# Performance work log

Hardware: AMD Instinct MI355X
Metric: run time of the kernel (lower is better)

## Reference

```python
import jax, jax.numpy as jnp
import numpy as np

N_NODES = 100000

def gcn_conv(x, W, b, src, dst, n_nodes):
    # x: [N, Fin], W: [Fin, Fout], b: [Fout]; src/dst include self-loops.
    h = x @ W                                            # [N, Fout]
    deg = jnp.zeros((n_nodes,), x.dtype).at[dst].add(1.0)  # in-degree incl. self-loop
    dinv = jax.lax.rsqrt(deg)                            # deg >= 1 due to self-loops
    norm = dinv[src] * dinv[dst]                         # [E']
    msg = h[src] * norm[:, None]                         # [E', Fout]
    out = jax.ops.segment_sum(msg, dst, num_segments=n_nodes)
    return out + b

def setup_inputs() -> dict:
    key = jax.random.key(0)
    k1, k2, k3, k4, k5, k6 = jax.random.split(key, 6)
    in_c, hid_c, out_c = 128, 64, 32
    x = jax.random.normal(k1, (N_NODES, in_c), dtype=jnp.float32)
    edge_index = jax.random.randint(k2, (2, 1600000), 0, N_NODES, dtype=jnp.int64)
    # Glorot-ish init for weights
    W1 = jax.random.normal(k3, (in_c, hid_c), dtype=jnp.float32) / np.sqrt(in_c)
    b1 = jnp.zeros((hid_c,), dtype=jnp.float32)
    W2 = jax.random.normal(k4, (hid_c, out_c), dtype=jnp.float32) / np.sqrt(hid_c)
    b2 = jnp.zeros((out_c,), dtype=jnp.float32)
    return {"x": x, "edge_index": edge_index, "W1": W1, "b1": b1, "W2": W2, "b2": b2}

def reference(x, edge_index, W1, b1, W2, b2):
    n = x.shape[0]
    loops = jnp.arange(n, dtype=edge_index.dtype)
    src = jnp.concatenate([edge_index[0], loops])   # add self-loops
    dst = jnp.concatenate([edge_index[1], loops])
    h = gcn_conv(x, W1, b1, src, dst, n)
    h = jax.nn.relu(h)
    out = gcn_conv(h, W2, b2, src, dst, n)
    return out
```

## Files before the change

kernel.cpp:

```cpp
#include <hip/hip_runtime.h>
#include <hip/hip_bf16.h>


#define FIN1 128
#define FOUT1 64
#define FOUT2 32
#define PAD 64
#define NPB 200
#define NBUCKET 500
#define CAP 4096
#define EPB 4096

typedef unsigned int uint;
typedef unsigned short ushort;
typedef __attribute__((ext_vector_type(8))) short bf16x8;
typedef __attribute__((ext_vector_type(4))) float f32x4;

__device__ __forceinline__ ushort f2bf(float f) {
    uint u = __float_as_uint(f);
    return (ushort)((u + 0x7fffu + ((u >> 16) & 1u)) >> 16);
}
__device__ __forceinline__ float bf2f(ushort b) {
    return __uint_as_float(((uint)b) << 16);
}


__global__ __launch_bounds__(256) void bin_edges(const int* __restrict__ src,
                                                 const int* __restrict__ dst,
                                                 int* __restrict__ cursors,
                                                 int* __restrict__ binned, int e) {
    __shared__ int s_hist[NBUCKET];
    __shared__ int s_base[NBUCKET];
    __shared__ int s_cur[NBUCKET];
    const int t = threadIdx.x;
    for (int i = t; i < NBUCKET; i += 256) s_hist[i] = 0;
    __syncthreads();
    const int base = blockIdx.x * EPB;
    int vpk[16], vb[16];
#pragma unroll
    for (int k = 0; k < 16; ++k) {
        int idx = base + t + k * 256;
        bool ok = idx < e;
        int s = ok ? src[idx] : 0;
        int d = ok ? dst[idx] : 0;
        int bk = d / NPB;
        vb[k] = ok ? bk : -1;
        vpk[k] = s | ((d - bk * NPB) << 17);
        if (ok) atomicAdd(&s_hist[bk], 1);
    }
    __syncthreads();
    for (int i = t; i < NBUCKET; i += 256) {
        int h = s_hist[i];
        s_base[i] = (h > 0) ? atomicAdd(&cursors[i], h) : 0;
        s_cur[i] = 0;
    }
    __syncthreads();
#pragma unroll
    for (int k = 0; k < 16; ++k) {
        int bk = vb[k];
        if (bk >= 0) {
            int r = s_base[bk] + atomicAdd(&s_cur[bk], 1);
            if (r < CAP) binned[(size_t)bk * CAP + r] = vpk[k];
        }
    }
}


__global__ __launch_bounds__(256) void build_ell(const int* __restrict__ binned,
                                                 const int* __restrict__ cursors,
                                                 int* __restrict__ counts,
                                                 float* __restrict__ dinv,
                                                 int* __restrict__ ell, int n) {
    __shared__ int s_cnt[NPB];
    __shared__ int s_ell[NPB * PAD];
    const int b = blockIdx.x, t = threadIdx.x;
    for (int i = t; i < NPB; i += 256) s_cnt[i] = 0;
    {
        int4 pv = make_int4(n, n, n, n);
        int4* s4 = (int4*)s_ell;
        for (int i = t; i < NPB * PAD / 4; i += 256) s4[i] = pv;
    }
    __syncthreads();
    const int len = min(cursors[b], CAP);
    const int* edges = binned + (size_t)b * CAP;
    const int node0 = b * NPB;
    for (int i = t; i < len; i += 256) {
        int pk = edges[i];
        int local = pk >> 17;
        int r = atomicAdd(&s_cnt[local], 1);
        if (r < PAD) s_ell[local * PAD + r] = pk & 0x1FFFF;
    }
    __syncthreads();
    for (int i = t; i < NPB; i += 256) {
        int node = node0 + i;
        if (node < n) {
            int full = s_cnt[i];
            counts[node] = min((full + 7) & ~7, PAD);
            dinv[node] = rsqrtf((float)full + 1.0f);
        }
    }
    int4* d4 = (int4*)(ell + (size_t)node0 * PAD);
    const int4* s4 = (const int4*)s_ell;
    for (int i = t; i < NPB * PAD / 4; i += 256) d4[i] = s4[i];
}

template <int K, int F, int CT, int LOG2F>
__device__ __forceinline__ void stage_W(const float* __restrict__ W, ushort* sB, int t) {
    for (int sidx = t; sidx < K * F; sidx += 256) {
        int k = sidx >> LOG2F;
        int f = sidx & (F - 1);
        int kc = k >> 5, j = k & 7, quadb = (k >> 3) & 3;
        int c = f >> 4, nn = f & 15;
        int d = ((kc * CT + c) * 64 + quadb * 16 + nn) * 8 + j;
        sB[d] = f2bf(W[sidx]);
    }
}


template <int K, int F, int LOG2F>
__global__ __launch_bounds__(256) void gemm_mfma(const float* __restrict__ A,
                                                 const float* __restrict__ W,
                                                 const float* __restrict__ dinv,
                                                 ushort* __restrict__ out, int n) {
    constexpr int KC = K / 32;
    constexpr int CT = F / 16;
    __shared__ ushort sB[KC * CT * 64 * 8];
    const int t = threadIdx.x;
    stage_W<K, F, CT, LOG2F>(W, sB, t);
    __syncthreads();

    const int w = threadIdx.x >> 6;
    const int lane = threadIdx.x & 63;
    const int quad = lane >> 4;
    const int mcol = lane & 15;

    bf16x8 bfr[KC][CT];
    const bf16x8* sB8 = reinterpret_cast<const bf16x8*>(sB);
#pragma unroll
    for (int kc = 0; kc < KC; ++kc)
#pragma unroll
        for (int c = 0; c < CT; ++c)
            bfr[kc][c] = sB8[(kc * CT + c) * 64 + lane];

    const int ntiles = n / 16;
#pragma unroll
    for (int tt = 0; tt < 2; ++tt) {
        const int tile = (blockIdx.x * 4 + w) * 2 + tt;
        if (tile >= ntiles) continue;
        const int rb = tile * 16;
        bf16x8 afr[KC];
#pragma unroll
        for (int kc = 0; kc < KC; ++kc) {
            const float* ap = A + (size_t)(rb + mcol) * K + kc * 32 + quad * 8;
            float4 x0 = *reinterpret_cast<const float4*>(ap);
            float4 x1 = *reinterpret_cast<const float4*>(ap + 4);
            bf16x8 a;
            a[0] = (short)f2bf(x0.x); a[1] = (short)f2bf(x0.y);
            a[2] = (short)f2bf(x0.z); a[3] = (short)f2bf(x0.w);
            a[4] = (short)f2bf(x1.x); a[5] = (short)f2bf(x1.y);
            a[6] = (short)f2bf(x1.z); a[7] = (short)f2bf(x1.w);
            afr[kc] = a;
        }
        f32x4 acc[CT];
#pragma unroll
        for (int c = 0; c < CT; ++c) acc[c] = (f32x4){0.f, 0.f, 0.f, 0.f};
#pragma unroll
        for (int kc = 0; kc < KC; ++kc)
#pragma unroll
            for (int c = 0; c < CT; ++c)
                acc[c] = __builtin_amdgcn_mfma_f32_16x16x32_bf16(afr[kc], bfr[kc][c], acc[c], 0, 0, 0);
        float dv[4];
#pragma unroll
        for (int r = 0; r < 4; ++r) dv[r] = dinv[rb + quad * 4 + r];
#pragma unroll
        for (int c = 0; c < CT; ++c)
#pragma unroll
            for (int r = 0; r < 4; ++r)
                out[(size_t)(rb + quad * 4 + r) * F + c * 16 + mcol] = f2bf(acc[c][r] * dv[r]);
    }
}


#define SASTRIDE 72

__global__ __launch_bounds__(256) void agg_gemm2(const ushort* __restrict__ h,
                                                 const int* __restrict__ counts,
                                                 const int* __restrict__ ell,
                                                 const float* __restrict__ dinv,
                                                 const float* __restrict__ bias,
                                                 const float* __restrict__ W2,
                                                 ushort* __restrict__ out, int n) {
    constexpr int KC = 2;
    constexpr int CT = 2;
    __shared__ ushort sB[KC * CT * 64 * 8];
    __shared__ ushort sA[16 * SASTRIDE];
    const int t = threadIdx.x;
    stage_W<64, 32, CT, 5>(W2, sB, t);

    const int w = __builtin_amdgcn_readfirstlane(t >> 6);
    const int lane = t & 63;
    const int rb = blockIdx.x * 16;
    const int node0 = rb + w * 4;

    int cnt[4];
    const int* rows[4];
    float acc[4];
#pragma unroll
    for (int i = 0; i < 4; ++i) {
        cnt[i] = counts[node0 + i];
        rows[i] = ell + (size_t)(node0 + i) * PAD;
        acc[i] = bf2f(h[(size_t)(node0 + i) * 64 + lane]);
    }
    const int cmax = max(max(cnt[0], cnt[1]), max(cnt[2], cnt[3]));
    for (int r = 0; r < cmax; r += 8) {
        float v[4][8];
#pragma unroll
        for (int i = 0; i < 4; ++i) {
            if (r < cnt[i]) {
#pragma unroll
                for (int u = 0; u < 8; ++u)
                    v[i][u] = bf2f(h[(size_t)rows[i][r + u] * 64 + lane]);
            }
        }
#pragma unroll
        for (int i = 0; i < 4; ++i) {
            if (r < cnt[i])
                acc[i] += ((v[i][0] + v[i][1]) + (v[i][2] + v[i][3])) +
                          ((v[i][4] + v[i][5]) + (v[i][6] + v[i][7]));
        }
    }
#pragma unroll
    for (int i = 0; i < 4; ++i) {
        float vv = fmaxf(acc[i] * dinv[node0 + i] + bias[lane], 0.0f);
        sA[(w * 4 + i) * SASTRIDE + lane] = f2bf(vv);
    }
    __syncthreads();

    if (w < 2) {
        const int quad = lane >> 4;
        const int mcol = lane & 15;
        const bf16x8* sB8 = reinterpret_cast<const bf16x8*>(sB);
        f32x4 acc2 = (f32x4){0.f, 0.f, 0.f, 0.f};
#pragma unroll
        for (int kc = 0; kc < KC; ++kc) {
            bf16x8 afr = *reinterpret_cast<const bf16x8*>(&sA[mcol * SASTRIDE + kc * 32 + quad * 8]);
            bf16x8 bfr = sB8[(kc * CT + w) * 64 + lane];
            acc2 = __builtin_amdgcn_mfma_f32_16x16x32_bf16(afr, bfr, acc2, 0, 0, 0);
        }
#pragma unroll
        for (int r = 0; r < 4; ++r) {
            int orow = rb + quad * 4 + r;
            out[(size_t)orow * 32 + w * 16 + mcol] = f2bf(acc2[r] * dinv[orow]);
        }
    }
}


__global__ __launch_bounds__(256) void aggregate32_bf(const ushort* __restrict__ h,
                                                      const int* __restrict__ counts,
                                                      const int* __restrict__ ell,
                                                      const float* __restrict__ dinv,
                                                      const float* __restrict__ bias,
                                                      float* __restrict__ out, int n) {
    const int wv = __builtin_amdgcn_readfirstlane(threadIdx.x >> 6);
    const int lane = threadIdx.x & 63;
    const int f = lane & 31;
    const int node0 = blockIdx.x * 16 + wv * 4;

    int cnt[4];
    const int* rows[4];
    float acc[4];
#pragma unroll
    for (int i = 0; i < 4; ++i) {
        cnt[i] = counts[node0 + i];
        rows[i] = ell + (size_t)(node0 + i) * PAD;
        acc[i] = bf2f(h[(size_t)(node0 + i) * 32 + f]);
    }
    const int cmax = max(max(cnt[0], cnt[1]), max(cnt[2], cnt[3]));
    for (int r = 0; r < cmax; r += 8) {
        float v[4][8];
#pragma unroll
        for (int i = 0; i < 4; ++i) {
            if (r < cnt[i]) {
#pragma unroll
                for (int u = 0; u < 8; ++u)
                    v[i][u] = bf2f(h[(size_t)rows[i][r + u] * 32 + f]);
            }
        }
#pragma unroll
        for (int i = 0; i < 4; ++i) {
            if (r < cnt[i])
                acc[i] += ((v[i][0] + v[i][1]) + (v[i][2] + v[i][3])) +
                          ((v[i][4] + v[i][5]) + (v[i][6] + v[i][7]));
        }
    }
    if (lane < 32) {
#pragma unroll
        for (int i = 0; i < 4; ++i)
            out[(size_t)(node0 + i) * 32 + f] = acc[i] * dinv[node0 + i] + bias[f];
    }
}

extern "C" void kernel_launch(void* const* d_in, const int* in_sizes, int n_in,
                              void* d_out, int out_size, void* d_ws, size_t ws_size,
                              hipStream_t stream) {
    const float* x  = (const float*)d_in[0];
    const int*   ei = (const int*)d_in[1];
    const float* W1 = (const float*)d_in[2];
    const float* b1 = (const float*)d_in[3];
    const float* W2 = (const float*)d_in[4];
    const float* b2 = (const float*)d_in[5];
    float* out = (float*)d_out;

    const int N = in_sizes[0] / FIN1;
    const int E = in_sizes[1] / 2;
    const int* src = ei;
    const int* dst = ei + E;

    char* w = (char*)d_ws;
    size_t off = 0;
    auto alloc = [&](size_t bytes) -> char* {
        char* p = w + off;
        off = (off + bytes + 255) & ~(size_t)255;
        return p;
    };
    int*    cursors = (int*)alloc((size_t)NBUCKET * 4);
    int*    counts  = (int*)alloc((size_t)N * 4);
    float*  dinv    = (float*)alloc((size_t)N * 4);
    int*    binned  = (int*)alloc((size_t)NBUCKET * CAP * 4);
    int*    ell     = (int*)alloc((size_t)N * PAD * 4);
    ushort* hbf     = (ushort*)alloc((size_t)(N + 1) * 64 * 2);
    ushort* h2bf    = (ushort*)alloc((size_t)(N + 1) * 32 * 2);
    (void)ws_size;

    const int BINB = (E + EPB - 1) / EPB;
    const int GB = (N / 16 + 7) / 8;
    const int FB = N / 16;
    const int AB = N / 16;

    hipMemsetAsync(cursors, 0, (size_t)NBUCKET * 4, stream);
    hipMemsetAsync(hbf + (size_t)N * 64, 0, 64 * 2, stream);
    hipMemsetAsync(h2bf + (size_t)N * 32, 0, 32 * 2, stream);
    bin_edges<<<BINB, 256, 0, stream>>>(src, dst, cursors, binned, E);
    build_ell<<<NBUCKET, 256, 0, stream>>>(binned, cursors, counts, dinv, ell, N);

    gemm_mfma<FIN1, FOUT1, 6><<<GB, 256, 0, stream>>>(x, W1, dinv, hbf, N);
    agg_gemm2<<<FB, 256, 0, stream>>>(hbf, counts, ell, dinv, b1, W2, h2bf, N);
    aggregate32_bf<<<AB, 256, 0, stream>>>(h2bf, counts, ell, dinv, b2, out, N);
}
```

Baseline: 228.7 us.

## Pack two nodes per wave in aggregation, prefetch ELL indices, use nontemporal memory ops

Both aggregation kernels now split each wave into two halves, each half serving a different node. In the 64-feature kernel each lane loads two bf16 values, and in the 32-feature kernel lanes that were idle now do work. ELL neighbour indices for the next chunk are prefetched into registers. The per-node `r < cnt` guard is dropped, which is safe because counts are padded to multiples of 8 with a dummy node. Several streaming loads and stores (binning, ELL build, GEMM A reads, final output) switch to nontemporal builtins to reduce cache pollution, at the cost of higher register pressure.

```diff
diff --git a/kernel.cpp b/kernel.cpp
--- a/kernel.cpp
+++ b/kernel.cpp
@@ -15,6 +15,7 @@
 typedef unsigned short ushort;
 typedef __attribute__((ext_vector_type(8))) short bf16x8;
 typedef __attribute__((ext_vector_type(4))) float f32x4;
+typedef __attribute__((ext_vector_type(4))) int i32x4;
 
 __device__ __forceinline__ ushort f2bf(float f) {
     uint u = __float_as_uint(f);
@@ -60,7 +61,7 @@
         int bk = vb[k];
         if (bk >= 0) {
             int r = s_base[bk] + atomicAdd(&s_cur[bk], 1);
-            if (r < CAP) binned[(size_t)bk * CAP + r] = vpk[k];
+            if (r < CAP) __builtin_nontemporal_store(vpk[k], &binned[(size_t)bk * CAP + r]);
         }
     }
 }
@@ -76,8 +77,8 @@
     const int b = blockIdx.x, t = threadIdx.x;
     for (int i = t; i < NPB; i += 256) s_cnt[i] = 0;
     {
-        int4 pv = make_int4(n, n, n, n);
-        int4* s4 = (int4*)s_ell;
+        i32x4 pv = (i32x4){n, n, n, n};
+        i32x4* s4 = (i32x4*)s_ell;
         for (int i = t; i < NPB * PAD / 4; i += 256) s4[i] = pv;
     }
     __syncthreads();
@@ -85,7 +86,7 @@
     const int* edges = binned + (size_t)b * CAP;
     const int node0 = b * NPB;
     for (int i = t; i < len; i += 256) {
-        int pk = edges[i];
+        int pk = __builtin_nontemporal_load(&edges[i]);
         int local = pk >> 17;
         int r = atomicAdd(&s_cnt[local], 1);
         if (r < PAD) s_ell[local * PAD + r] = pk & 0x1FFFF;
@@ -99,9 +100,9 @@
             dinv[node] = rsqrtf((float)full + 1.0f);
         }
     }
-    int4* d4 = (int4*)(ell + (size_t)node0 * PAD);
-    const int4* s4 = (const int4*)s_ell;
-    for (int i = t; i < NPB * PAD / 4; i += 256) d4[i] = s4[i];
+    i32x4* d4 = (i32x4*)(ell + (size_t)node0 * PAD);
+    const i32x4* s4 = (const i32x4*)s_ell;
+    for (int i = t; i < NPB * PAD / 4; i += 256) __builtin_nontemporal_store(s4[i], &d4[i]);
 }
 
 template <int K, int F, int CT, int LOG2F>
@@ -152,13 +153,13 @@
 #pragma unroll
         for (int kc = 0; kc < KC; ++kc) {
             const float* ap = A + (size_t)(rb + mcol) * K + kc * 32 + quad * 8;
-            float4 x0 = *reinterpret_cast<const float4*>(ap);
-            float4 x1 = *reinterpret_cast<const float4*>(ap + 4);
+            f32x4 x0 = __builtin_nontemporal_load(reinterpret_cast<const f32x4*>(ap));
+            f32x4 x1 = __builtin_nontemporal_load(reinterpret_cast<const f32x4*>(ap + 4));
             bf16x8 a;
-            a[0] = (short)f2bf(x0.x); a[1] = (short)f2bf(x0.y);
-            a[2] = (short)f2bf(x0.z); a[3] = (short)f2bf(x0.w);
-            a[4] = (short)f2bf(x1.x); a[5] = (short)f2bf(x1.y);
-            a[6] = (short)f2bf(x1.z); a[7] = (short)f2bf(x1.w);
+            a[0] = (short)f2bf(x0[0]); a[1] = (short)f2bf(x0[1]);
+            a[2] = (short)f2bf(x0[2]); a[3] = (short)f2bf(x0[3]);
+            a[4] = (short)f2bf(x1[0]); a[5] = (short)f2bf(x1[1]);
+            a[6] = (short)f2bf(x1[2]); a[7] = (short)f2bf(x1[3]);
             afr[kc] = a;
         }
         f32x4 acc[CT];
@@ -199,40 +200,76 @@
 
     const int w = __builtin_amdgcn_readfirstlane(t >> 6);
     const int lane = t & 63;
+    const int half = lane >> 5;
+    const int fl = lane & 31;
     const int rb = blockIdx.x * 16;
     const int node0 = rb + w * 4;
 
     int cnt[4];
     const int* rows[4];
-    float acc[4];
 #pragma unroll
     for (int i = 0; i < 4; ++i) {
         cnt[i] = counts[node0 + i];
         rows[i] = ell + (size_t)(node0 + i) * PAD;
-        acc[i] = bf2f(h[(size_t)(node0 + i) * 64 + lane]);
+    }
+    float accx[2], accy[2];
+#pragma unroll
+    for (int p = 0; p < 2; ++p) {
+        int node = node0 + 2 * p + half;
+        ushort2 sv = *reinterpret_cast<const ushort2*>(h + (((uint)node << 6) + (fl << 1)));
+        accx[p] = bf2f(sv.x); accy[p] = bf2f(sv.y);
     }
     const int cmax = max(max(cnt[0], cnt[1]), max(cnt[2], cnt[3]));
+    int iA[2][8], iB[2][8];
+#pragma unroll
+    for (int p = 0; p < 2; ++p)
+#pragma unroll
+        for (int u = 0; u < 8; ++u) { iA[p][u] = rows[2 * p][u]; iB[p][u] = rows[2 * p + 1][u]; }
+
     for (int r = 0; r < cmax; r += 8) {
-        float v[4][8];
-#pragma unroll
-        for (int i = 0; i < 4; ++i) {
-            if (r < cnt[i]) {
-#pragma unroll
-                for (int u = 0; u < 8; ++u)
-                    v[i][u] = bf2f(h[(size_t)rows[i][r + u] * 64 + lane]);
+        const bool more = (r + 8) < cmax;
+        int nA[2][8], nB[2][8];
+        if (more) {
+#pragma unroll
+            for (int p = 0; p < 2; ++p)
+#pragma unroll
+                for (int u = 0; u < 8; ++u) {
+                    nA[p][u] = rows[2 * p][r + 8 + u];
+                    nB[p][u] = rows[2 * p + 1][r + 8 + u];
+                }
+        }
+        float vx[2][8], vy[2][8];
+#pragma unroll
+        for (int p = 0; p < 2; ++p)
+#pragma unroll
+            for (int u = 0; u < 8; ++u) {
+                int idx = half ? iB[p][u] : iA[p][u];
+                ushort2 g = *reinterpret_cast<const ushort2*>(h + (((uint)idx << 6) + (fl << 1)));
+                vx[p][u] = bf2f(g.x); vy[p][u] = bf2f(g.y);
             }
-        }
-#pragma unroll
-        for (int i = 0; i < 4; ++i) {
-            if (r < cnt[i])
-                acc[i] += ((v[i][0] + v[i][1]) + (v[i][2] + v[i][3])) +
-                          ((v[i][4] + v[i][5]) + (v[i][6] + v[i][7]));
-        }
-    }
-#pragma unroll
-    for (int i = 0; i < 4; ++i) {
-        float vv = fmaxf(acc[i] * dinv[node0 + i] + bias[lane], 0.0f);
-        sA[(w * 4 + i) * SASTRIDE + lane] = f2bf(vv);
+#pragma unroll
+        for (int p = 0; p < 2; ++p) {
+            accx[p] += ((vx[p][0] + vx[p][1]) + (vx[p][2] + vx[p][3])) +
+                       ((vx[p][4] + vx[p][5]) + (vx[p][6] + vx[p][7]));
+            accy[p] += ((vy[p][0] + vy[p][1]) + (vy[p][2] + vy[p][3])) +
+                       ((vy[p][4] + vy[p][5]) + (vy[p][6] + vy[p][7]));
+        }
+        if (more) {
+#pragma unroll
+            for (int p = 0; p < 2; ++p)
+#pragma unroll
+                for (int u = 0; u < 8; ++u) { iA[p][u] = nA[p][u]; iB[p][u] = nB[p][u]; }
+        }
+    }
+#pragma unroll
+    for (int p = 0; p < 2; ++p) {
+        int node = node0 + 2 * p + half;
+        float dv = dinv[node];
+        float2 bv = *reinterpret_cast<const float2*>(bias + (fl << 1));
+        float r0 = fmaxf(accx[p] * dv + bv.x, 0.0f);
+        float r1 = fmaxf(accy[p] * dv + bv.y, 0.0f);
+        ushort2 o; o.x = f2bf(r0); o.y = f2bf(r1);
+        *reinterpret_cast<ushort2*>(&sA[(w * 4 + 2 * p + half) * SASTRIDE + (fl << 1)]) = o;
     }
     __syncthreads();
 
@@ -264,40 +301,66 @@
                                                       float* __restrict__ out, int n) {
     const int wv = __builtin_amdgcn_readfirstlane(threadIdx.x >> 6);
     const int lane = threadIdx.x & 63;
-    const int f = lane & 31;
+    const int half = lane >> 5;
+    const int fl = lane & 31;
     const int node0 = blockIdx.x * 16 + wv * 4;
 
     int cnt[4];
     const int* rows[4];
-    float acc[4];
 #pragma unroll
     for (int i = 0; i < 4; ++i) {
         cnt[i] = counts[node0 + i];
         rows[i] = ell + (size_t)(node0 + i) * PAD;
-        acc[i] = bf2f(h[(size_t)(node0 + i) * 32 + f]);
+    }
+    float acc[2];
+#pragma unroll
+    for (int p = 0; p < 2; ++p) {
+        int node = node0 + 2 * p + half;
+        acc[p] = bf2f(h[((uint)node << 5) + fl]);
     }
     const int cmax = max(max(cnt[0], cnt[1]), max(cnt[2], cnt[3]));
+    int iA[2][8], iB[2][8];
+#pragma unroll
+    for (int p = 0; p < 2; ++p)
+#pragma unroll
+        for (int u = 0; u < 8; ++u) { iA[p][u] = rows[2 * p][u]; iB[p][u] = rows[2 * p + 1][u]; }
+
     for (int r = 0; r < cmax; r += 8) {
-        float v[4][8];
-#pragma unroll
-        for (int i = 0; i < 4; ++i) {
-            if (r < cnt[i]) {
-#pragma unroll
-                for (int u = 0; u < 8; ++u)
-                    v[i][u] = bf2f(h[(size_t)rows[i][r + u] * 32 + f]);
+        const bool more = (r + 8) < cmax;
+        int nA[2][8], nB[2][8];
+        if (more) {
+#pragma unroll
+            for (int p = 0; p < 2; ++p)
+#pragma unroll
+                for (int u = 0; u < 8; ++u) {
+                    nA[p][u] = rows[2 * p][r + 8 + u];
+                    nB[p][u] = rows[2 * p + 1][r + 8 + u];
+                }
+        }
+        float v[2][8];
+#pragma unroll
+        for (int p = 0; p < 2; ++p)
+#pragma unroll
+            for (int u = 0; u < 8; ++u) {
+                int idx = half ? iB[p][u] : iA[p][u];
+                v[p][u] = bf2f(h[((uint)idx << 5) + fl]);
             }
-        }
-#pragma unroll
-        for (int i = 0; i < 4; ++i) {
-            if (r < cnt[i])
-                acc[i] += ((v[i][0] + v[i][1]) + (v[i][2] + v[i][3])) +
-                          ((v[i][4] + v[i][5]) + (v[i][6] + v[i][7]));
-        }
-    }
-    if (lane < 32) {
-#pragma unroll
-        for (int i = 0; i < 4; ++i)
-            out[(size_t)(node0 + i) * 32 + f] = acc[i] * dinv[node0 + i] + bias[f];
+#pragma unroll
+        for (int p = 0; p < 2; ++p)
+            acc[p] += ((v[p][0] + v[p][1]) + (v[p][2] + v[p][3])) +
+                      ((v[p][4] + v[p][5]) + (v[p][6] + v[p][7]));
+        if (more) {
+#pragma unroll
+            for (int p = 0; p < 2; ++p)
+#pragma unroll
+                for (int u = 0; u < 8; ++u) { iA[p][u] = nA[p][u]; iB[p][u] = nB[p][u]; }
+        }
+    }
+#pragma unroll
+    for (int p = 0; p < 2; ++p) {
+        int node = node0 + 2 * p + half;
+        float o = acc[p] * dinv[node] + bias[fl];
+        __builtin_nontemporal_store(o, &out[((uint)node << 5) + fl]);
     }
 }
 
```

Measured after the change: 248.0 us. +8.5%, slower.

## Remap aggregation lanes to gather 4-wide bf16 vectors per node with index prefetch

Applied to the files above, without the earlier changes.

Both aggregation kernels now assign each 16-lane (or 8-lane) group of a wavefront to one of four nodes, so each lane gathers 4 contiguous bf16 features per neighbor. Previously every lane gathered a single element for all four nodes. Neighbor indices for the next chunk are prefetched one iteration ahead, and the 32-wide kernel splits the neighbor chunks across half-waves and reduces them with a shuffle. Nontemporal loads and stores are also added in build_ell and the first GEMM. This reduces the number of gather instructions and improves per-load width, at the cost of more registers and per-node divergence inside a wavefront. Padded entries pointing at row n are still read, so h must hold a valid zero row at index n.

```diff
diff --git a/kernel.cpp b/kernel.cpp
--- a/kernel.cpp
+++ b/kernel.cpp
@@ -14,7 +14,9 @@
 typedef unsigned int uint;
 typedef unsigned short ushort;
 typedef __attribute__((ext_vector_type(8))) short bf16x8;
+typedef __attribute__((ext_vector_type(4))) ushort u16x4;
 typedef __attribute__((ext_vector_type(4))) float f32x4;
+typedef __attribute__((ext_vector_type(4))) int i32x4;
 
 __device__ __forceinline__ ushort f2bf(float f) {
     uint u = __float_as_uint(f);
@@ -76,8 +78,8 @@
     const int b = blockIdx.x, t = threadIdx.x;
     for (int i = t; i < NPB; i += 256) s_cnt[i] = 0;
     {
-        int4 pv = make_int4(n, n, n, n);
-        int4* s4 = (int4*)s_ell;
+        i32x4 pv = (i32x4){n, n, n, n};
+        i32x4* s4 = (i32x4*)s_ell;
         for (int i = t; i < NPB * PAD / 4; i += 256) s4[i] = pv;
     }
     __syncthreads();
@@ -85,7 +87,7 @@
     const int* edges = binned + (size_t)b * CAP;
     const int node0 = b * NPB;
     for (int i = t; i < len; i += 256) {
-        int pk = edges[i];
+        int pk = __builtin_nontemporal_load(&edges[i]);
         int local = pk >> 17;
         int r = atomicAdd(&s_cnt[local], 1);
         if (r < PAD) s_ell[local * PAD + r] = pk & 0x1FFFF;
@@ -99,9 +101,9 @@
             dinv[node] = rsqrtf((float)full + 1.0f);
         }
     }
-    int4* d4 = (int4*)(ell + (size_t)node0 * PAD);
-    const int4* s4 = (const int4*)s_ell;
-    for (int i = t; i < NPB * PAD / 4; i += 256) d4[i] = s4[i];
+    i32x4* d4 = (i32x4*)(ell + (size_t)node0 * PAD);
+    const i32x4* s4 = (const i32x4*)s_ell;
+    for (int i = t; i < NPB * PAD / 4; i += 256) __builtin_nontemporal_store(s4[i], &d4[i]);
 }
 
 template <int K, int F, int CT, int LOG2F>
@@ -152,13 +154,13 @@
 #pragma unroll
         for (int kc = 0; kc < KC; ++kc) {
             const float* ap = A + (size_t)(rb + mcol) * K + kc * 32 + quad * 8;
-            float4 x0 = *reinterpret_cast<const float4*>(ap);
-            float4 x1 = *reinterpret_cast<const float4*>(ap + 4);
+            f32x4 x0 = __builtin_nontemporal_load(reinterpret_cast<const f32x4*>(ap));
+            f32x4 x1 = __builtin_nontemporal_load(reinterpret_cast<const f32x4*>(ap + 4));
             bf16x8 a;
-            a[0] = (short)f2bf(x0.x); a[1] = (short)f2bf(x0.y);
-            a[2] = (short)f2bf(x0.z); a[3] = (short)f2bf(x0.w);
-            a[4] = (short)f2bf(x1.x); a[5] = (short)f2bf(x1.y);
-            a[6] = (short)f2bf(x1.z); a[7] = (short)f2bf(x1.w);
+            a[0] = (short)f2bf(x0[0]); a[1] = (short)f2bf(x0[1]);
+            a[2] = (short)f2bf(x0[2]); a[3] = (short)f2bf(x0[3]);
+            a[4] = (short)f2bf(x1[0]); a[5] = (short)f2bf(x1[1]);
+            a[6] = (short)f2bf(x1[2]); a[7] = (short)f2bf(x1[3]);
             afr[kc] = a;
         }
         f32x4 acc[CT];
@@ -199,40 +201,71 @@
 
     const int w = __builtin_amdgcn_readfirstlane(t >> 6);
     const int lane = t & 63;
+    const int q = lane >> 4;
+    const int fi = (lane & 15) * 4;
+    const bool qb0 = (q & 1) != 0;
+    const bool qb1 = (q & 2) != 0;
     const int rb = blockIdx.x * 16;
     const int node0 = rb + w * 4;
 
-    int cnt[4];
-    const int* rows[4];
-    float acc[4];
-#pragma unroll
-    for (int i = 0; i < 4; ++i) {
-        cnt[i] = counts[node0 + i];
-        rows[i] = ell + (size_t)(node0 + i) * PAD;
-        acc[i] = bf2f(h[(size_t)(node0 + i) * 64 + lane]);
-    }
-    const int cmax = max(max(cnt[0], cnt[1]), max(cnt[2], cnt[3]));
+    const int* __restrict__ r0 = ell + (size_t)(node0 + 0) * PAD;
+    const int* __restrict__ r1 = ell + (size_t)(node0 + 1) * PAD;
+    const int* __restrict__ r2 = ell + (size_t)(node0 + 2) * PAD;
+    const int* __restrict__ r3 = ell + (size_t)(node0 + 3) * PAD;
+    const int cmax = max(max(counts[node0 + 0], counts[node0 + 1]),
+                         max(counts[node0 + 2], counts[node0 + 3]));
+
+    f32x4 accA = (f32x4){0.f, 0.f, 0.f, 0.f};
+    f32x4 accB = (f32x4){0.f, 0.f, 0.f, 0.f};
+    {
+        u16x4 sv = *reinterpret_cast<const u16x4*>(h + (((uint)(node0 + q)) << 6) + fi);
+        f32x4 g;
+        g[0] = bf2f(sv[0]); g[1] = bf2f(sv[1]); g[2] = bf2f(sv[2]); g[3] = bf2f(sv[3]);
+        accA += g;
+    }
+
+    int i0[8], i1[8], i2[8], i3[8];
+#pragma unroll
+    for (int u = 0; u < 8; ++u) { i0[u] = r0[u]; i1[u] = r1[u]; i2[u] = r2[u]; i3[u] = r3[u]; }
+
     for (int r = 0; r < cmax; r += 8) {
-        float v[4][8];
-#pragma unroll
-        for (int i = 0; i < 4; ++i) {
-            if (r < cnt[i]) {
-#pragma unroll
-                for (int u = 0; u < 8; ++u)
-                    v[i][u] = bf2f(h[(size_t)rows[i][r + u] * 64 + lane]);
+        const bool more = (r + 8) < cmax;
+        int n0[8], n1[8], n2[8], n3[8];
+        if (more) {
+#pragma unroll
+            for (int u = 0; u < 8; ++u) {
+                n0[u] = r0[r + 8 + u]; n1[u] = r1[r + 8 + u];
+                n2[u] = r2[r + 8 + u]; n3[u] = r3[r + 8 + u];
             }
         }
-#pragma unroll
-        for (int i = 0; i < 4; ++i) {
-            if (r < cnt[i])
-                acc[i] += ((v[i][0] + v[i][1]) + (v[i][2] + v[i][3])) +
-                          ((v[i][4] + v[i][5]) + (v[i][6] + v[i][7]));
-        }
-    }
-#pragma unroll
-    for (int i = 0; i < 4; ++i) {
-        float vv = fmaxf(acc[i] * dinv[node0 + i] + bias[lane], 0.0f);
-        sA[(w * 4 + i) * SASTRIDE + lane] = f2bf(vv);
+        u16x4 v[8];
+#pragma unroll
+        for (int u = 0; u < 8; ++u) {
+            int idx = qb1 ? (qb0 ? i3[u] : i2[u]) : (qb0 ? i1[u] : i0[u]);
+            v[u] = *reinterpret_cast<const u16x4*>(h + (((uint)idx) << 6) + fi);
+        }
+#pragma unroll
+        for (int u = 0; u < 8; ++u) {
+            f32x4 g;
+            g[0] = bf2f(v[u][0]); g[1] = bf2f(v[u][1]);
+            g[2] = bf2f(v[u][2]); g[3] = bf2f(v[u][3]);
+            if (u & 1) accB += g; else accA += g;
+        }
+        if (more) {
+#pragma unroll
+            for (int u = 0; u < 8; ++u) { i0[u] = n0[u]; i1[u] = n1[u]; i2[u] = n2[u]; i3[u] = n3[u]; }
+        }
+    }
+    {
+        float d0 = dinv[node0 + 0], d1 = dinv[node0 + 1];
+        float d2 = dinv[node0 + 2], d3 = dinv[node0 + 3];
+        float dv = qb1 ? (qb0 ? d3 : d2) : (qb0 ? d1 : d0);
+        f32x4 bv = *reinterpret_cast<const f32x4*>(bias + fi);
+        f32x4 acc = accA + accB;
+        u16x4 o;
+#pragma unroll
+        for (int j = 0; j < 4; ++j) o[j] = f2bf(fmaxf(acc[j] * dv + bv[j], 0.0f));
+        *reinterpret_cast<u16x4*>(&sA[(w * 4 + q) * SASTRIDE + fi]) = o;
     }
     __syncthreads();
 
@@ -264,40 +297,74 @@
                                                       float* __restrict__ out, int n) {
     const int wv = __builtin_amdgcn_readfirstlane(threadIdx.x >> 6);
     const int lane = threadIdx.x & 63;
-    const int f = lane & 31;
+    const int s = lane >> 3;
+    const int q = s & 3;
+    const int e = s >> 2;
+    const int fi = (lane & 7) * 4;
+    const bool qb0 = (q & 1) != 0;
+    const bool qb1 = (q & 2) != 0;
+    const bool eb  = e != 0;
     const int node0 = blockIdx.x * 16 + wv * 4;
 
-    int cnt[4];
-    const int* rows[4];
-    float acc[4];
-#pragma unroll
-    for (int i = 0; i < 4; ++i) {
-        cnt[i] = counts[node0 + i];
-        rows[i] = ell + (size_t)(node0 + i) * PAD;
-        acc[i] = bf2f(h[(size_t)(node0 + i) * 32 + f]);
-    }
-    const int cmax = max(max(cnt[0], cnt[1]), max(cnt[2], cnt[3]));
+    const int* __restrict__ r0 = ell + (size_t)(node0 + 0) * PAD;
+    const int* __restrict__ r1 = ell + (size_t)(node0 + 1) * PAD;
+    const int* __restrict__ r2 = ell + (size_t)(node0 + 2) * PAD;
+    const int* __restrict__ r3 = ell + (size_t)(node0 + 3) * PAD;
+    const int cmax = max(max(counts[node0 + 0], counts[node0 + 1]),
+                         max(counts[node0 + 2], counts[node0 + 3]));
+
+    f32x4 acc = (f32x4){0.f, 0.f, 0.f, 0.f};
+    if (e == 0) {
+        u16x4 sv = *reinterpret_cast<const u16x4*>(h + (((uint)(node0 + q)) << 5) + fi);
+        f32x4 g;
+        g[0] = bf2f(sv[0]); g[1] = bf2f(sv[1]); g[2] = bf2f(sv[2]); g[3] = bf2f(sv[3]);
+        acc += g;
+    }
+
+    int i0[8], i1[8], i2[8], i3[8];
+#pragma unroll
+    for (int u = 0; u < 8; ++u) { i0[u] = r0[u]; i1[u] = r1[u]; i2[u] = r2[u]; i3[u] = r3[u]; }
+
     for (int r = 0; r < cmax; r += 8) {
-        float v[4][8];
-#pragma unroll
-        for (int i = 0; i < 4; ++i) {
-            if (r < cnt[i]) {
-#pragma unroll
-                for (int u = 0; u < 8; ++u)
-                    v[i][u] = bf2f(h[(size_t)rows[i][r + u] * 32 + f]);
+        const bool more = (r + 8) < cmax;
+        int n0[8], n1[8], n2[8], n3[8];
+        if (more) {
+#pragma unroll
+            for (int u = 0; u < 8; ++u) {
+                n0[u] = r0[r + 8 + u]; n1[u] = r1[r + 8 + u];
+                n2[u] = r2[r + 8 + u]; n3[u] = r3[r + 8 + u];
             }
         }
-#pragma unroll
-        for (int i = 0; i < 4; ++i) {
-            if (r < cnt[i])
-                acc[i] += ((v[i][0] + v[i][1]) + (v[i][2] + v[i][3])) +
-                          ((v[i][4] + v[i][5]) + (v[i][6] + v[i][7]));
-        }
-    }
-    if (lane < 32) {
-#pragma unroll
-        for (int i = 0; i < 4; ++i)
-            out[(size_t)(node0 + i) * 32 + f] = acc[i] * dinv[node0 + i] + bias[f];
+        u16x4 v[4];
+#pragma unroll
+        for (int u = 0; u < 8; u += 2) {
+            int ilo = qb1 ? (qb0 ? i3[u] : i2[u]) : (qb0 ? i1[u] : i0[u]);
+            int ihi = qb1 ? (qb0 ? i3[u + 1] : i2[u + 1]) : (qb0 ? i1[u + 1] : i0[u + 1]);
+            int idx = eb ? ihi : ilo;
+            v[u >> 1] = *reinterpret_cast<const u16x4*>(h + (((uint)idx) << 5) + fi);
+        }
+#pragma unroll
+        for (int u = 0; u < 4; ++u) {
+            f32x4 g;
+            g[0] = bf2f(v[u][0]); g[1] = bf2f(v[u][1]);
+            g[2] = bf2f(v[u][2]); g[3] = bf2f(v[u][3]);
+            acc += g;
+        }
+        if (more) {
+#pragma unroll
+            for (int u = 0; u < 8; ++u) { i0[u] = n0[u]; i1[u] = n1[u]; i2[u] = n2[u]; i3[u] = n3[u]; }
+        }
+    }
+#pragma unroll
+    for (int j = 0; j < 4; ++j) acc[j] += __shfl_xor(acc[j], 32, 64);
+
+    if (e == 0) {
+        float d0 = dinv[node0 + 0], d1 = dinv[node0 + 1];
+        float d2 = dinv[node0 + 2], d3 = dinv[node0 + 3];
+        float dv = qb1 ? (qb0 ? d3 : d2) : (qb0 ? d1 : d0);
+        f32x4 bv = *reinterpret_cast<const f32x4*>(bias + fi);
+        f32x4 o = acc * dv + bv;
+        __builtin_nontemporal_store(o, reinterpret_cast<f32x4*>(out + (((uint)(node0 + q)) << 5) + fi));
     }
 }
 
```

Measured after the change: 219.2 us. 4.2% less time.
